# Optimization experiments

Hardware: AMD Instinct MI355X
Metric: run time of the kernel (lower is better)

Reference implementation:

```python
import jax, jax.numpy as jnp
import numpy as np

B, H, W, C, UNITS = 16, 64, 64, 64, 128

def setup_inputs() -> dict:
    key = jax.random.key(0)
    k1, k2 = jax.random.split(key)
    x = jax.random.normal(k1, (B, H, W, C), dtype=jnp.float32)
    # 'random_normal' keras initializer defaults to stddev=0.05
    w = jax.random.normal(k2, (UNITS, C, W, H), dtype=jnp.float32) * 0.05
    return {"x": x, "w": w}

def reference(x, w):
    # Original: transpose NHWC->NCHW, broadcasted matmul (W,H)@(H,W),
    # reduce-sum over C, transpose back, relu.
    # Fused contraction: y[b,i,j,u] = sum_{c,h} w[u,c,i,h] * x[b,h,j,c]
    y = jnp.einsum('ucih,bhjc->biju', w, x)  # (B, W, W, units)
    return jax.nn.relu(y)
```

## Files before the change

kernel.cpp:

```cpp
#include <hip/hip_runtime.h>
#include <hip/hip_bf16.h>


typedef __attribute__((ext_vector_type(4))) float f32x4;
typedef __attribute__((ext_vector_type(8))) short bf16x8;
typedef __attribute__((ext_vector_type(4))) unsigned int u32x4;
typedef __attribute__((ext_vector_type(2))) unsigned int u32x2;
typedef unsigned short ushort_t;

static __device__ __forceinline__ unsigned int cvt_pk_bf16(float lo, float hi) {
  unsigned int r;
  asm("v_cvt_pk_bf16_f32 %0, %1, %2" : "=v"(r) : "v"(lo), "v"(hi));
  return r;
}

static __device__ __forceinline__ void async_copy16(void* lds, const void* g) {
  __builtin_amdgcn_global_load_lds(
      (const __attribute__((address_space(1))) unsigned int*)g,
      (__attribute__((address_space(3))) unsigned int*)lds, 16, 0, 0);
}

__global__ __launch_bounds__(256)
void conv_x(const float* __restrict__ X, ushort_t* __restrict__ Xb, int n4) {
  int idx = blockIdx.x * 256 + threadIdx.x;
  const int stride = gridDim.x * 256;
  for (; idx < n4; idx += stride) {
    f32x4 v = ((const f32x4*)X)[idx];
    u32x2 o;
    o.x = cvt_pk_bf16(v.x, v.y);
    o.y = cvt_pk_bf16(v.z, v.w);
    ((u32x2*)Xb)[idx] = o;
  }
}

__global__ __launch_bounds__(256)
void conv_w(const float* __restrict__ W, ushort_t* __restrict__ Wb) {
  __shared__ float T[64][65];
  const int bid = blockIdx.x;
  const int u = bid >> 6;
  const int i = bid & 63;
  const int t = threadIdx.x;

  const int hq = t & 15;
  const int c4 = t >> 4;
  const float* base = W + (((size_t)u * 64) * 64 + i) * 64;
#pragma unroll
  for (int it = 0; it < 4; ++it) {
    const int c = it * 16 + c4;
    f32x4 v = *(const f32x4*)(base + (size_t)c * 4096 + hq * 4);
    *(f32x4*)&T[c][hq * 4] = v;
  }
  __syncthreads();

  const int h = t >> 2;
  const int c0 = (t & 3) * 16;
  unsigned int pk[8];
#pragma unroll
  for (int q = 0; q < 8; ++q)
    pk[q] = cvt_pk_bf16(T[c0 + 2 * q][h], T[c0 + 2 * q + 1][h]);
  ushort_t* out = Wb + (((size_t)i * 128 + u) * 64 + h) * 64 + c0;
  ((u32x4*)out)[0] = *(u32x4*)&pk[0];
  ((u32x4*)out)[1] = *(u32x4*)&pk[4];
}

__global__ __launch_bounds__(512, 2)
void gemm8(const ushort_t* __restrict__ Xb, const ushort_t* __restrict__ Wb,
           float* __restrict__ O) {
  __shared__ ushort_t As[3][128 * 64];
  __shared__ ushort_t Bs[3][256 * 64];

  const int tid = threadIdx.x;
  const int lane = tid & 63;
  const int wid = tid >> 6;
  const int wm = wid >> 2;
  const int wn = wid & 3;

  const int bid = blockIdx.x;
  const int wg = (bid & 7) * 32 + (bid >> 3);
  const int mt = wg & 7;
  const int nt2 = wg >> 3;

  const char* XbB = (const char*)Xb;
  const char* WbB = (const char*)Wb;

  int a_dst[2]; size_t a_src[2];
#pragma unroll
  for (int it = 0; it < 2; ++it) {
    const int flat = it * 8192 + tid * 16;
    const int row = flat >> 7;
    const int p = (flat >> 4) & 7;
    const int b = mt * 2 + (row >> 6);
    const int j = row & 63;
    a_dst[it] = flat;
    a_src[it] = (size_t)b * 524288 + (size_t)j * 128 + ((p ^ (row & 7)) << 4);
  }
  int b_dst[4]; size_t b_src[4];
#pragma unroll
  for (int it = 0; it < 4; ++it) {
    const int flat = it * 8192 + tid * 16;
    const int nl = flat >> 7;
    const int p = (flat >> 4) & 7;
    b_dst[it] = flat;
    b_src[it] = (size_t)(nt2 * 256 + nl) * 8192 + ((p ^ (nl & 7)) << 4);
  }

  int a_ro[2][4], b_ro[2][4];
#pragma unroll
  for (int kk = 0; kk < 2; ++kk) {
#pragma unroll
    for (int f = 0; f < 4; ++f) {
      int row = wm * 64 + f * 16 + (lane & 15);
      int byte0 = row * 128 + kk * 64 + (lane >> 4) * 16;
      a_ro[kk][f] = byte0 ^ ((row & 7) << 4);
      row = wn * 64 + f * 16 + (lane & 15);
      byte0 = row * 128 + kk * 64 + (lane >> 4) * 16;
      b_ro[kk][f] = byte0 ^ ((row & 7) << 4);
    }
  }

  f32x4 acc[4][4];
#pragma unroll
  for (int i = 0; i < 4; ++i)
#pragma unroll
    for (int j = 0; j < 4; ++j) acc[i][j] = (f32x4){0.f, 0.f, 0.f, 0.f};

  auto stage = [&](int buf, int h) {
    char* la = (char*)&As[buf][0];
    char* lb = (char*)&Bs[buf][0];
#pragma unroll
    for (int it = 0; it < 2; ++it)
      async_copy16(la + a_dst[it], XbB + a_src[it] + (size_t)h * 8192);
#pragma unroll
    for (int it = 0; it < 4; ++it)
      async_copy16(lb + b_dst[it], WbB + b_src[it] + (size_t)h * 128);
  };

  stage(0, 0);
  stage(1, 1);
  asm volatile("s_waitcnt vmcnt(6)" ::: "memory");
  __builtin_amdgcn_s_barrier();

  int cur = 0, pre = 2;
  for (int t = 0; t < 64; ++t) {
    const int h2 = t + 2;
    const char* ab = (const char*)&As[cur][0];
    const char* bb = (const char*)&Bs[cur][0];

    if (h2 < 64) stage(pre, h2);

    bf16x8 af[2][4], bfr[2][4];
#pragma unroll
    for (int kk = 0; kk < 2; ++kk) {
#pragma unroll
      for (int f = 0; f < 4; ++f) af[kk][f] = *(const bf16x8*)(ab + a_ro[kk][f]);
#pragma unroll
      for (int f = 0; f < 4; ++f) bfr[kk][f] = *(const bf16x8*)(bb + b_ro[kk][f]);
    }
#pragma unroll
    for (int kk = 0; kk < 2; ++kk)
#pragma unroll
      for (int mf = 0; mf < 4; ++mf)
#pragma unroll
        for (int nf = 0; nf < 4; ++nf)
          acc[mf][nf] = __builtin_amdgcn_mfma_f32_16x16x32_bf16(
              af[kk][mf], bfr[kk][nf], acc[mf][nf], 0, 0, 0);

    asm volatile("s_waitcnt lgkmcnt(0)" ::: "memory");
    if (t < 62) {
      asm volatile("s_waitcnt vmcnt(6)" ::: "memory");
    } else {
      asm volatile("s_waitcnt vmcnt(0)" ::: "memory");
    }
    __builtin_amdgcn_s_barrier();

    cur = (cur == 2) ? 0 : cur + 1;
    pre = (pre == 2) ? 0 : pre + 1;
  }

  const int rbase = (lane >> 4) * 4;
  const int cn = lane & 15;
#pragma unroll
  for (int mf = 0; mf < 4; ++mf) {
#pragma unroll
    for (int r = 0; r < 4; ++r) {
      const int ml = wm * 64 + mf * 16 + rbase + r;
      const int m = mt * 128 + ml;
      const int b = m >> 6;
      const int j = m & 63;
#pragma unroll
      for (int nf = 0; nf < 4; ++nf) {
        const int nloc = wn * 64 + nf * 16 + cn;
        const int i = nt2 * 2 + (nloc >> 7);
        const int u = nloc & 127;
        O[(((size_t)b * 64 + i) * 64 + j) * 128 + u] = fmaxf(acc[mf][nf][r], 0.f);
      }
    }
  }
}

__global__ __launch_bounds__(256, 2)
void fused_gemm(const float* __restrict__ X, const float* __restrict__ Wt,
                float* __restrict__ O) {
  __shared__ ushort_t As[2][128 * 64];
  __shared__ ushort_t Bs[2][128 * 64];
  const int tid = threadIdx.x;
  const int lane = tid & 63;
  const int wid = tid >> 6;
  const int wm = wid >> 1;
  const int wn = wid & 1;
  const int bid = blockIdx.x;
  const int wg = (bid & 7) * 64 + (bid >> 3);
  const int mt = wg & 7;
  const int nt = wg >> 3;
  const int a_ml = tid >> 1;
  const int a_hp = (tid & 1) * 2;
  const int a_b = (mt * 128 + a_ml) >> 6;
  const int a_j = a_ml & 63;
  const float* a_base = X + ((size_t)a_b << 18) + ((size_t)a_j << 6);
  const int b_nl = tid >> 1;
  const int b_c8 = (tid & 1) * 8;
  const float* b_base = Wt + ((size_t)b_nl << 18) + ((size_t)nt << 6);
  f32x4 ra[2][4];
  f32x4 rb[8];
  f32x4 acc[4][4];
#pragma unroll
  for (int i = 0; i < 4; ++i)
#pragma unroll
    for (int j = 0; j < 4; ++j) acc[i][j] = (f32x4){0.f, 0.f, 0.f, 0.f};
  auto stage_load = [&](int t) {
    const int th = t & 15;
    const int tc = t >> 4;
    const int c0 = tc * 16;
    const int h0 = th * 4;
#pragma unroll
    for (int s = 0; s < 2; ++s) {
      const float* p = a_base + (size_t)(h0 + a_hp + s) * 4096 + c0;
#pragma unroll
      for (int q = 0; q < 4; ++q) ra[s][q] = ((const f32x4*)p)[q];
    }
#pragma unroll
    for (int q = 0; q < 8; ++q)
      rb[q] = *(const f32x4*)(b_base + (size_t)(c0 + b_c8 + q) * 4096 + h0);
  };
  auto stage_write = [&](int buf) {
    char* abase = (char*)&As[buf][0];
    const int swa = (a_ml & 7) << 4;
#pragma unroll
    for (int s = 0; s < 2; ++s) {
      u32x4 lo, hi;
      lo.x = cvt_pk_bf16(ra[s][0].x, ra[s][0].y);
      lo.y = cvt_pk_bf16(ra[s][0].z, ra[s][0].w);
      lo.z = cvt_pk_bf16(ra[s][1].x, ra[s][1].y);
      lo.w = cvt_pk_bf16(ra[s][1].z, ra[s][1].w);
      hi.x = cvt_pk_bf16(ra[s][2].x, ra[s][2].y);
      hi.y = cvt_pk_bf16(ra[s][2].z, ra[s][2].w);
      hi.z = cvt_pk_bf16(ra[s][3].x, ra[s][3].y);
      hi.w = cvt_pk_bf16(ra[s][3].z, ra[s][3].w);
      const int byte0 = a_ml * 128 + (a_hp + s) * 32;
      *(u32x4*)(abase + (byte0 ^ swa)) = lo;
      *(u32x4*)(abase + ((byte0 + 16) ^ swa)) = hi;
    }
    char* bbase = (char*)&Bs[buf][0];
    const int swb = (b_nl & 7) << 4;
#pragma unroll
    for (int hl = 0; hl < 4; ++hl) {
      u32x4 v;
      v.x = cvt_pk_bf16(rb[0][hl], rb[1][hl]);
      v.y = cvt_pk_bf16(rb[2][hl], rb[3][hl]);
      v.z = cvt_pk_bf16(rb[4][hl], rb[5][hl]);
      v.w = cvt_pk_bf16(rb[6][hl], rb[7][hl]);
      const int byte0 = b_nl * 128 + (hl * 16 + b_c8) * 2;
      *(u32x4*)(bbase + (byte0 ^ swb)) = v;
    }
  };
  auto compute = [&](int buf) {
    const char* abase = (const char*)&As[buf][0];
    const char* bbase = (const char*)&Bs[buf][0];
#pragma unroll
    for (int kk = 0; kk < 2; ++kk) {
      bf16x8 af[4], bfr[4];
#pragma unroll
      for (int mf = 0; mf < 4; ++mf) {
        const int row = wm * 64 + mf * 16 + (lane & 15);
        const int byte0 = row * 128 + kk * 64 + (lane >> 4) * 16;
        af[mf] = *(const bf16x8*)(abase + (byte0 ^ ((row & 7) << 4)));
      }
#pragma unroll
      for (int nf = 0; nf < 4; ++nf) {
        const int row = wn * 64 + nf * 16 + (lane & 15);
        const int byte0 = row * 128 + kk * 64 + (lane >> 4) * 16;
        bfr[nf] = *(const bf16x8*)(bbase + (byte0 ^ ((row & 7) << 4)));
      }
#pragma unroll
      for (int mf = 0; mf < 4; ++mf)
#pragma unroll
        for (int nf = 0; nf < 4; ++nf)
          acc[mf][nf] = __builtin_amdgcn_mfma_f32_16x16x32_bf16(
              af[mf], bfr[nf], acc[mf][nf], 0, 0, 0);
    }
  };
  stage_load(0);
  stage_write(0);
  __syncthreads();
  int cur = 0;
  for (int t = 0; t < 64; ++t) {
    if (t + 1 < 64) stage_load(t + 1);
    compute(cur);
    if (t + 1 < 64) stage_write(cur ^ 1);
    __syncthreads();
    cur ^= 1;
  }
  const int rbase = (lane >> 4) * 4;
  const int cn = lane & 15;
#pragma unroll
  for (int mf = 0; mf < 4; ++mf) {
#pragma unroll
    for (int r = 0; r < 4; ++r) {
      const int ml = wm * 64 + mf * 16 + rbase + r;
      const int m = mt * 128 + ml;
      const int b = m >> 6;
      const int j = m & 63;
      float* orow = O + (((size_t)b * 64 + nt) * 64 + j) * 128;
#pragma unroll
      for (int nf = 0; nf < 4; ++nf) {
        const int u = wn * 64 + nf * 16 + cn;
        orow[u] = fmaxf(acc[mf][nf][r], 0.f);
      }
    }
  }
}

extern "C" void kernel_launch(void* const* d_in, const int* in_sizes, int n_in,
                              void* d_out, int out_size, void* d_ws, size_t ws_size,
                              hipStream_t stream) {
  const float* x = (const float*)d_in[0];
  const float* w = (const float*)d_in[1];
  float* out = (float*)d_out;

  const size_t XB_BYTES = (size_t)16 * 64 * 64 * 64 * 2;
  const size_t WB_BYTES = (size_t)64 * 128 * 64 * 64 * 2;

  if (ws_size >= XB_BYTES + WB_BYTES) {
    ushort_t* Xb = (ushort_t*)d_ws;
    ushort_t* Wb = (ushort_t*)((char*)d_ws + XB_BYTES);
    hipLaunchKernelGGL(conv_x, dim3(1024), dim3(256), 0, stream, x, Xb,
                       (int)(16 * 64 * 64 * 64 / 4));
    hipLaunchKernelGGL(conv_w, dim3(8192), dim3(256), 0, stream, w, Wb);
    hipLaunchKernelGGL(gemm8, dim3(256), dim3(512), 0, stream, Xb, Wb, out);
  } else {
    hipLaunchKernelGGL(fused_gemm, dim3(512), dim3(256), 0, stream, x, w, out);
  }
}
```

Measured before the change: 125.0 us.

## Load A operand directly to registers, shrink tile, split K-step with priority hints

Replaces the 512-thread 128x256 GEMM tile with a 256-thread 128x128 tile over twice as many workgroups. The A (activation) operand is no longer staged through LDS; it is loaded straight from global memory into registers and double-buffered one step ahead, so only B uses the LDS ring. Each K-step is split into two half-steps with extra barriers and s_setprio around the MFMA blocks, which interleaves LDS reads and async copies with compute. This cuts LDS traffic and footprint but adds uncoalesced-ish global reads for A, more barriers per step, and halves the B reuse per tile.

```diff
diff --git a/kernel.cpp b/kernel.cpp
--- a/kernel.cpp
+++ b/kernel.cpp
@@ -63,60 +63,49 @@
   ((u32x4*)out)[1] = *(u32x4*)&pk[4];
 }
 
-__global__ __launch_bounds__(512, 2)
-void gemm8(const ushort_t* __restrict__ Xb, const ushort_t* __restrict__ Wb,
+__global__ __launch_bounds__(256, 2)
+void gemm4(const ushort_t* __restrict__ Xb, const ushort_t* __restrict__ Wb,
            float* __restrict__ O) {
-  __shared__ ushort_t As[3][128 * 64];
-  __shared__ ushort_t Bs[3][256 * 64];
+  __shared__ ushort_t Bs[3][128 * 64];
 
   const int tid = threadIdx.x;
   const int lane = tid & 63;
   const int wid = tid >> 6;
-  const int wm = wid >> 2;
-  const int wn = wid & 3;
+  const int wm = wid >> 1;
+  const int wn = wid & 1;
 
   const int bid = blockIdx.x;
-  const int wg = (bid & 7) * 32 + (bid >> 3);
+  const int wg = (bid & 7) * 64 + (bid >> 3);
   const int mt = wg & 7;
-  const int nt2 = wg >> 3;
-
-  const char* XbB = (const char*)Xb;
+  const int nt = wg >> 3;
+
   const char* WbB = (const char*)Wb;
 
-  int a_dst[2]; size_t a_src[2];
-#pragma unroll
-  for (int it = 0; it < 2; ++it) {
-    const int flat = it * 8192 + tid * 16;
-    const int row = flat >> 7;
-    const int p = (flat >> 4) & 7;
-    const int b = mt * 2 + (row >> 6);
-    const int j = row & 63;
-    a_dst[it] = flat;
-    a_src[it] = (size_t)b * 524288 + (size_t)j * 128 + ((p ^ (row & 7)) << 4);
-  }
   int b_dst[4]; size_t b_src[4];
 #pragma unroll
   for (int it = 0; it < 4; ++it) {
-    const int flat = it * 8192 + tid * 16;
+    const int flat = it * 4096 + tid * 16;
     const int nl = flat >> 7;
     const int p = (flat >> 4) & 7;
     b_dst[it] = flat;
-    b_src[it] = (size_t)(nt2 * 256 + nl) * 8192 + ((p ^ (nl & 7)) << 4);
-  }
-
-  int a_ro[2][4], b_ro[2][4];
-#pragma unroll
-  for (int kk = 0; kk < 2; ++kk) {
+    b_src[it] = (size_t)(nt * 128 + nl) * 8192 + ((p ^ (nl & 7)) << 4);
+  }
+
+  int b_ro[2][4];
+#pragma unroll
+  for (int kk = 0; kk < 2; ++kk)
 #pragma unroll
     for (int f = 0; f < 4; ++f) {
-      int row = wm * 64 + f * 16 + (lane & 15);
-      int byte0 = row * 128 + kk * 64 + (lane >> 4) * 16;
-      a_ro[kk][f] = byte0 ^ ((row & 7) << 4);
-      row = wn * 64 + f * 16 + (lane & 15);
-      byte0 = row * 128 + kk * 64 + (lane >> 4) * 16;
+      const int row = wn * 64 + f * 16 + (lane & 15);
+      const int byte0 = row * 128 + kk * 64 + (lane >> 4) * 16;
       b_ro[kk][f] = byte0 ^ ((row & 7) << 4);
     }
-  }
+
+  size_t a_g[4];
+#pragma unroll
+  for (int mf = 0; mf < 4; ++mf)
+    a_g[mf] = (size_t)(mt * 2 + wm) * 262144 +
+              (size_t)(mf * 16 + (lane & 15)) * 64 + (lane >> 4) * 8;
 
   f32x4 acc[4][4];
 #pragma unroll
@@ -125,56 +114,77 @@
     for (int j = 0; j < 4; ++j) acc[i][j] = (f32x4){0.f, 0.f, 0.f, 0.f};
 
   auto stage = [&](int buf, int h) {
-    char* la = (char*)&As[buf][0];
     char* lb = (char*)&Bs[buf][0];
-#pragma unroll
-    for (int it = 0; it < 2; ++it)
-      async_copy16(la + a_dst[it], XbB + a_src[it] + (size_t)h * 8192);
 #pragma unroll
     for (int it = 0; it < 4; ++it)
       async_copy16(lb + b_dst[it], WbB + b_src[it] + (size_t)h * 128);
   };
 
-  stage(0, 0);
-  stage(1, 1);
-  asm volatile("s_waitcnt vmcnt(6)" ::: "memory");
-  __builtin_amdgcn_s_barrier();
-
+  auto loadA = [&](bf16x8 (&ar)[4][2], int t) {
+#pragma unroll
+    for (int mf = 0; mf < 4; ++mf)
+#pragma unroll
+      for (int kk = 0; kk < 2; ++kk)
+        ar[mf][kk] = *(const bf16x8*)(Xb + a_g[mf] + (size_t)t * 4096 + kk * 32);
+  };
+
+  bf16x8 aA[4][2], aB[4][2];
   int cur = 0, pre = 2;
-  for (int t = 0; t < 64; ++t) {
-    const int h2 = t + 2;
-    const char* ab = (const char*)&As[cur][0];
+
+  auto step = [&](int t, bf16x8 (&aC)[4][2], bf16x8 (&aN)[4][2]) {
     const char* bb = (const char*)&Bs[cur][0];
-
-    if (h2 < 64) stage(pre, h2);
-
-    bf16x8 af[2][4], bfr[2][4];
-#pragma unroll
-    for (int kk = 0; kk < 2; ++kk) {
-#pragma unroll
-      for (int f = 0; f < 4; ++f) af[kk][f] = *(const bf16x8*)(ab + a_ro[kk][f]);
-#pragma unroll
-      for (int f = 0; f < 4; ++f) bfr[kk][f] = *(const bf16x8*)(bb + b_ro[kk][f]);
-    }
-#pragma unroll
-    for (int kk = 0; kk < 2; ++kk)
-#pragma unroll
-      for (int mf = 0; mf < 4; ++mf)
-#pragma unroll
-        for (int nf = 0; nf < 4; ++nf)
-          acc[mf][nf] = __builtin_amdgcn_mfma_f32_16x16x32_bf16(
-              af[kk][mf], bfr[kk][nf], acc[mf][nf], 0, 0, 0);
-
+    __builtin_amdgcn_sched_barrier(0);
+    if (t + 1 < 64) loadA(aN, t + 1);
+    bf16x8 bfr0[4];
+#pragma unroll
+    for (int f = 0; f < 4; ++f) bfr0[f] = *(const bf16x8*)(bb + b_ro[0][f]);
+    __builtin_amdgcn_s_barrier();
+    __builtin_amdgcn_s_setprio(1);
+#pragma unroll
+    for (int mf = 0; mf < 4; ++mf)
+#pragma unroll
+      for (int nf = 0; nf < 4; ++nf)
+        acc[mf][nf] = __builtin_amdgcn_mfma_f32_16x16x32_bf16(
+            aC[mf][0], bfr0[nf], acc[mf][nf], 0, 0, 0);
+    __builtin_amdgcn_s_setprio(0);
+    __builtin_amdgcn_s_barrier();
+
+    __builtin_amdgcn_sched_barrier(0);
+    bf16x8 bfr1[4];
+#pragma unroll
+    for (int f = 0; f < 4; ++f) bfr1[f] = *(const bf16x8*)(bb + b_ro[1][f]);
+    asm volatile("" ::: "memory");
+    if (t + 2 < 64) stage(pre, t + 2);
+    __builtin_amdgcn_s_barrier();
+    __builtin_amdgcn_s_setprio(1);
+#pragma unroll
+    for (int mf = 0; mf < 4; ++mf)
+#pragma unroll
+      for (int nf = 0; nf < 4; ++nf)
+        acc[mf][nf] = __builtin_amdgcn_mfma_f32_16x16x32_bf16(
+            aC[mf][1], bfr1[nf], acc[mf][nf], 0, 0, 0);
+    __builtin_amdgcn_s_setprio(0);
     asm volatile("s_waitcnt lgkmcnt(0)" ::: "memory");
     if (t < 62) {
-      asm volatile("s_waitcnt vmcnt(6)" ::: "memory");
-    } else {
+      asm volatile("s_waitcnt vmcnt(4)" ::: "memory");
+    } else if (t == 62) {
       asm volatile("s_waitcnt vmcnt(0)" ::: "memory");
     }
     __builtin_amdgcn_s_barrier();
-
     cur = (cur == 2) ? 0 : cur + 1;
     pre = (pre == 2) ? 0 : pre + 1;
+  };
+
+  stage(0, 0);
+  loadA(aA, 0);
+  asm volatile("" ::: "memory");
+  stage(1, 1);
+  asm volatile("s_waitcnt vmcnt(4)" ::: "memory");
+  __builtin_amdgcn_s_barrier();
+
+  for (int t = 0; t < 64; t += 2) {
+    step(t, aA, aB);
+    step(t + 1, aB, aA);
   }
 
   const int rbase = (lane >> 4) * 4;
@@ -187,12 +197,11 @@
       const int m = mt * 128 + ml;
       const int b = m >> 6;
       const int j = m & 63;
+      float* orow = O + (((size_t)b * 64 + nt) * 64 + j) * 128;
 #pragma unroll
       for (int nf = 0; nf < 4; ++nf) {
-        const int nloc = wn * 64 + nf * 16 + cn;
-        const int i = nt2 * 2 + (nloc >> 7);
-        const int u = nloc & 127;
-        O[(((size_t)b * 64 + i) * 64 + j) * 128 + u] = fmaxf(acc[mf][nf][r], 0.f);
+        const int u = wn * 64 + nf * 16 + cn;
+        orow[u] = fmaxf(acc[mf][nf][r], 0.f);
       }
     }
   }
@@ -346,7 +355,7 @@
     hipLaunchKernelGGL(conv_x, dim3(1024), dim3(256), 0, stream, x, Xb,
                        (int)(16 * 64 * 64 * 64 / 4));
     hipLaunchKernelGGL(conv_w, dim3(8192), dim3(256), 0, stream, w, Wb);
-    hipLaunchKernelGGL(gemm8, dim3(256), dim3(512), 0, stream, Xb, Wb, out);
+    hipLaunchKernelGGL(gemm4, dim3(512), dim3(256), 0, stream, Xb, Wb, out);
   } else {
     hipLaunchKernelGGL(fused_gemm, dim3(512), dim3(256), 0, stream, x, w, out);
   }
```

Measured after the change: 179.3 us. +43.5%, slower.
